# Kernel tuning notes

Hardware: AMD Instinct MI355X
Metric: run time of the kernel (lower is better)

The kernel has to match this reference:

```python
import jax, jax.numpy as jnp
import numpy as np

N_NODES = 100000
N_EDGES = 1600000
IN_F, HID, N_CLASS = 128, 128, 40


def setup_inputs() -> dict:
    key = jax.random.key(0)
    ks = jax.random.split(key, 12)
    feat = jax.random.normal(ks[0], (N_NODES, IN_F), dtype=jnp.float32)
    src = jax.random.randint(ks[1], (N_EDGES,), 0, N_NODES, dtype=jnp.int32)
    dst = jax.random.randint(ks[2], (N_EDGES,), 0, N_NODES, dtype=jnp.int32)
    s = 1.0 / np.sqrt(IN_F)
    W1_self = jax.random.uniform(ks[3], (IN_F, HID), minval=-s, maxval=s)
    W1_neigh = jax.random.uniform(ks[4], (IN_F, HID), minval=-s, maxval=s)
    b1 = jnp.zeros((HID,), jnp.float32)
    s2 = 1.0 / np.sqrt(HID)
    W2_self = jax.random.uniform(ks[5], (HID, HID), minval=-s2, maxval=s2)
    W2_neigh = jax.random.uniform(ks[6], (HID, HID), minval=-s2, maxval=s2)
    b2 = jnp.zeros((HID,), jnp.float32)
    W_score = jax.random.uniform(ks[7], (HID, N_CLASS), minval=-s2, maxval=s2)
    b_score = jax.random.uniform(ks[8], (N_CLASS,), minval=-s2, maxval=s2)
    return {"feat": feat, "src": src, "dst": dst,
            "W1_self": W1_self, "W1_neigh": W1_neigh, "b1": b1,
            "W2_self": W2_self, "W2_neigh": W2_neigh, "b2": b2,
            "W_score": W_score, "b_score": b_score}


def _mean_agg(h, src, dst, deg_inv):
    # gather -> segment-sum over destination nodes -> mean
    msg = h[src]                                              # [E, d]
    agg = jax.ops.segment_sum(msg, dst, num_segments=N_NODES)  # [N, d]
    return agg * deg_inv[:, None]


def _sage_conv(h, src, dst, deg_inv, W_self, W_neigh, b):
    h_neigh = _mean_agg(h, src, dst, deg_inv)
    return h @ W_self + h_neigh @ W_neigh + b


def reference(feat, src, dst, W1_self, W1_neigh, b1, W2_self, W2_neigh, b2, W_score, b_score):
    # dgl.add_self_loop: append (i, i) edges
    loops = jnp.arange(N_NODES, dtype=src.dtype)
    src_f = jnp.concatenate([src, loops])
    dst_f = jnp.concatenate([dst, loops])
    deg = jax.ops.segment_sum(jnp.ones_like(dst_f, dtype=feat.dtype), dst_f, num_segments=N_NODES)
    deg_inv = 1.0 / deg  # every node has a self loop -> deg >= 1
    h = _sage_conv(feat, src_f, dst_f, deg_inv, W1_self, W1_neigh, b1)
    h = jnp.where(h >= 0, h, 0.01 * h)  # LeakyReLU(0.01)
    h = _sage_conv(h, src_f, dst_f, deg_inv, W2_self, W2_neigh, b2)
    return h @ W_score + b_score
```

## Files before the change

### kernel.cpp

```cpp
#include <hip/hip_runtime.h>
#include <cstdint>
#include <cstddef>

#define N_NODES 100000
#define N_EDGES 1600000
#define FDIM 128
#define NCLS 40
#define SCAN_BLOCKS 98

#define FILL_CLASSES 8
#define FILL_BPC 256
#define FILL_EPB 6250
#define NODES_PER_CLASS (N_NODES / FILL_CLASSES)

__global__ void count_kernel(const int* __restrict__ dst, int* __restrict__ cnt, int E) {
    int e = blockIdx.x * blockDim.x + threadIdx.x;
    if (e < E) atomicAdd(&cnt[dst[e]], 1);
}

__global__ void scan_phase1(const int* __restrict__ cnt, int* __restrict__ excl,
                            int* __restrict__ bsum, float* __restrict__ deg_inv, int n) {
    __shared__ int lds[1024];
    int tid = threadIdx.x;
    int i = blockIdx.x * 1024 + tid;
    int v = (i < n) ? cnt[i] : 0;
    if (i < n) deg_inv[i] = 1.0f / (float)(v + 1);
    lds[tid] = v;
    __syncthreads();
    for (int d = 1; d < 1024; d <<= 1) {
        int t = (tid >= d) ? lds[tid - d] : 0;
        __syncthreads();
        lds[tid] += t;
        __syncthreads();
    }
    if (i < n) excl[i] = lds[tid] - v;
    if (tid == 1023) bsum[blockIdx.x] = lds[1023];
}

__global__ void scan_phase2(const int* __restrict__ bsum, int* __restrict__ boff, int nb) {
    __shared__ int lds[128];
    int tid = threadIdx.x;
    int v = (tid < nb) ? bsum[tid] : 0;
    lds[tid] = v;
    __syncthreads();
    for (int d = 1; d < 128; d <<= 1) {
        int t = (tid >= d) ? lds[tid - d] : 0;
        __syncthreads();
        lds[tid] += t;
        __syncthreads();
    }
    if (tid < nb) boff[tid] = lds[tid] - v;
    if (tid == 127) boff[nb] = lds[127];
}

__global__ void scan_phase3(const int* __restrict__ excl, const int* __restrict__ boff,
                            int* __restrict__ off, int n, int nb) {
    int i = blockIdx.x * blockDim.x + threadIdx.x;
    if (i < n) off[i] = excl[i] + boff[i >> 10];
    if (i == 0) off[n] = boff[nb];
}

__global__ __launch_bounds__(256) void fill_kernel(
        const int* __restrict__ src, const int* __restrict__ dst,
        const int* __restrict__ off, int* __restrict__ cnt,
        int* __restrict__ csr_src, int E) {
    int cls = blockIdx.x & (FILL_CLASSES - 1);
    int w   = blockIdx.x >> 3;
    int lo  = cls * NODES_PER_CLASS;
    int hi  = lo + NODES_PER_CLASS;
    int beg = w * FILL_EPB;
    int end = beg + FILL_EPB; if (end > E) end = E;
    for (int e = beg + threadIdx.x; e < end; e += 256) {
        int d = dst[e];
        if (d >= lo && d < hi) {
            int p = atomicSub(&cnt[d], 1) - 1;
            csr_src[off[d] + p] = src[e];
        }
    }
}

__global__ __launch_bounds__(256) void agg_kernel(
        const float* __restrict__ x, const int* __restrict__ csr_off,
        const int* __restrict__ csr_src, const float* __restrict__ deg_inv,
        float* __restrict__ outbuf, int N) {
    int wid = blockIdx.x * 4 + (threadIdx.x >> 6);
    int lane = threadIdx.x & 63;
    if (wid >= N) return;
    float2 acc = *((const float2*)(x + (size_t)wid * FDIM) + lane);
    int beg = csr_off[wid], end = csr_off[wid + 1];
    for (int j = beg; j < end; j += 64) {
        int c = end - j; if (c > 64) c = 64;
        int idx = (lane < c) ? csr_src[j + lane] : 0;
        int t = 0;
        for (; t + 16 <= c; t += 16) {
            float2 v[16];
#pragma unroll
            for (int u = 0; u < 16; ++u)
                v[u] = *((const float2*)(x + (size_t)__shfl(idx, t + u) * FDIM) + lane);
#pragma unroll
            for (int u = 0; u < 16; ++u) { acc.x += v[u].x; acc.y += v[u].y; }
        }
        for (; t + 4 <= c; t += 4) {
            float2 v[4];
#pragma unroll
            for (int u = 0; u < 4; ++u)
                v[u] = *((const float2*)(x + (size_t)__shfl(idx, t + u) * FDIM) + lane);
#pragma unroll
            for (int u = 0; u < 4; ++u) { acc.x += v[u].x; acc.y += v[u].y; }
        }
        for (; t < c; ++t) {
            float2 v = *((const float2*)(x + (size_t)__shfl(idx, t) * FDIM) + lane);
            acc.x += v.x; acc.y += v.y;
        }
    }
    float di = deg_inv[wid];
    float2 r; r.x = acc.x * di; r.y = acc.y * di;
    *((float2*)(outbuf + (size_t)wid * FDIM) + lane) = r;
}

__global__ __launch_bounds__(256) void gemm1_kernel(
        const float* __restrict__ feat, const float* __restrict__ agg,
        const float* __restrict__ Wself, const float* __restrict__ Wneigh,
        const float* __restrict__ bias, float* __restrict__ h1, int M) {
    __shared__ float At[32][132];
    __shared__ float Ws[32][132];
    int tid = threadIdx.x;
    int tx = tid & 15;
    int ty = tid >> 4;
    int row0 = blockIdx.x * 128;
    float acc[8][8];
#pragma unroll
    for (int i = 0; i < 8; ++i)
#pragma unroll
        for (int j = 0; j < 8; ++j) acc[i][j] = 0.f;

    for (int chunk = 0; chunk < 8; ++chunk) {
        const float* Asrc = (chunk < 4) ? feat : agg;
        const float* Wsrc = (chunk < 4) ? Wself : Wneigh;
        int kb = (chunk & 3) << 5;
        {
            int r = tid >> 1;
            int c0 = (tid & 1) << 4;
            int gr = row0 + r;
            const float* sp = Asrc + (size_t)gr * FDIM + kb + c0;
#pragma unroll
            for (int i = 0; i < 4; ++i) {
                float4 v = (gr < M) ? *(const float4*)(sp + (i << 2))
                                    : make_float4(0.f, 0.f, 0.f, 0.f);
                At[c0 + (i << 2) + 0][r] = v.x;
                At[c0 + (i << 2) + 1][r] = v.y;
                At[c0 + (i << 2) + 2][r] = v.z;
                At[c0 + (i << 2) + 3][r] = v.w;
            }
        }
        {
            int kr = tid >> 3;
            int c0 = (tid & 7) << 4;
            const float* sp = Wsrc + (size_t)(kb + kr) * FDIM + c0;
#pragma unroll
            for (int i = 0; i < 4; ++i)
                *(float4*)&Ws[kr][c0 + (i << 2)] = *(const float4*)(sp + (i << 2));
        }
        __syncthreads();
#pragma unroll 2
        for (int k = 0; k < 32; ++k) {
            float a[8], w[8];
            *(float4*)&a[0] = *(const float4*)&At[k][ty << 3];
            *(float4*)&a[4] = *(const float4*)&At[k][(ty << 3) + 4];
            *(float4*)&w[0] = *(const float4*)&Ws[k][tx << 3];
            *(float4*)&w[4] = *(const float4*)&Ws[k][(tx << 3) + 4];
#pragma unroll
            for (int i = 0; i < 8; ++i)
#pragma unroll
                for (int j = 0; j < 8; ++j)
                    acc[i][j] = fmaf(a[i], w[j], acc[i][j]);
        }
        __syncthreads();
    }
    float bcol[8];
    *(float4*)&bcol[0] = *(const float4*)&bias[tx << 3];
    *(float4*)&bcol[4] = *(const float4*)&bias[(tx << 3) + 4];
#pragma unroll
    for (int i = 0; i < 8; ++i) {
        int gr = row0 + (ty << 3) + i;
        if (gr < M) {
            float o[8];
#pragma unroll
            for (int j = 0; j < 8; ++j) {
                float v = acc[i][j] + bcol[j];
                o[j] = (v >= 0.f) ? v : 0.01f * v;
            }
            float4* dp = (float4*)(h1 + (size_t)gr * FDIM + (tx << 3));
            dp[0] = make_float4(o[0], o[1], o[2], o[3]);
            dp[1] = make_float4(o[4], o[5], o[6], o[7]);
        }
    }
}

__global__ void wfuse_kernel(const float* __restrict__ W2s, const float* __restrict__ W2n,
                             const float* __restrict__ b2, const float* __restrict__ Wsc,
                             const float* __restrict__ bsc,
                             float* __restrict__ Wf, float* __restrict__ bf) {
    int gid = blockIdx.x * blockDim.x + threadIdx.x;
    if (gid < 256 * NCLS) {
        int r = gid / NCLS, c = gid % NCLS;
        const float* wrow = (r < 128) ? (W2s + (size_t)r * 128) : (W2n + (size_t)(r - 128) * 128);
        float acc = 0.f;
        for (int k = 0; k < 128; ++k) acc = fmaf(wrow[k], Wsc[k * NCLS + c], acc);
        Wf[gid] = acc;
    } else if (gid < 256 * NCLS + NCLS) {
        int c = gid - 256 * NCLS;
        float acc = bsc[c];
        for (int k = 0; k < 128; ++k) acc = fmaf(b2[k], Wsc[k * NCLS + c], acc);
        bf[c] = acc;
    }
}

__global__ __launch_bounds__(256) void gemm2p_kernel(
        const float* __restrict__ h1, const float* __restrict__ Wf,
        float* __restrict__ pp, int M) {
    __shared__ float As[128][36];
    __shared__ float Ws2[32][84];
    int tid = threadIdx.x;
    int tx = tid & 7;
    int ty = tid >> 3;
    int row0 = blockIdx.x * 128;
    float acc[4][10];
#pragma unroll
    for (int i = 0; i < 4; ++i)
#pragma unroll
        for (int j = 0; j < 10; ++j) acc[i][j] = 0.f;

    for (int chunk = 0; chunk < 4; ++chunk) {
        int kb = chunk << 5;
        {
            int r = tid >> 1;
            int c0 = (tid & 1) << 4;
            int gr = row0 + r;
            const float* sp = h1 + (size_t)gr * FDIM + kb + c0;
#pragma unroll
            for (int i = 0; i < 4; ++i) {
                float4 v = (gr < M) ? *(const float4*)(sp + (i << 2))
                                    : make_float4(0.f, 0.f, 0.f, 0.f);
                *(float4*)&As[r][c0 + (i << 2)] = v;
            }
        }
        {
            for (int idx = tid; idx < 32 * 80; idx += 256) {
                int kr = idx / 80, c = idx % 80;
                float v = (c < NCLS) ? Wf[(kb + kr) * NCLS + c]
                                     : Wf[(128 + kb + kr) * NCLS + (c - NCLS)];
                Ws2[kr][c] = v;
            }
        }
        __syncthreads();
#pragma unroll 4
        for (int k = 0; k < 32; ++k) {
            float a[4], w[10];
#pragma unroll
            for (int i = 0; i < 4; ++i) a[i] = As[ty + (i << 5)][k];
#pragma unroll
            for (int j = 0; j < 10; ++j) w[j] = Ws2[k][tx + (j << 3)];
#pragma unroll
            for (int i = 0; i < 4; ++i)
#pragma unroll
                for (int j = 0; j < 10; ++j)
                    acc[i][j] = fmaf(a[i], w[j], acc[i][j]);
        }
        __syncthreads();
    }
#pragma unroll
    for (int i = 0; i < 4; ++i) {
        int gr = row0 + ty + (i << 5);
        if (gr < M) {
            float* dp = pp + (size_t)gr * 80 + tx;
#pragma unroll
            for (int j = 0; j < 10; ++j)
                dp[j << 3] = acc[i][j];
        }
    }
}

__global__ __launch_bounds__(256) void final_kernel(
        const float* __restrict__ pp, const int* __restrict__ csr_off,
        const int* __restrict__ csr_src, const float* __restrict__ deg_inv,
        const float* __restrict__ bf, float* __restrict__ out, int N) {
    int wid = blockIdx.x * 4 + (threadIdx.x >> 6);
    int lane = threadIdx.x & 63;
    if (wid >= N) return;
    bool act = (lane < NCLS);
    int ln = act ? lane : 0;
    float accv = act ? pp[(size_t)wid * 80 + NCLS + ln] : 0.f;
    int beg = csr_off[wid], end = csr_off[wid + 1];
    for (int j = beg; j < end; j += 64) {
        int c = end - j; if (c > 64) c = 64;
        int idx = (lane < c) ? csr_src[j + lane] : 0;
        int t = 0;
        for (; t + 16 <= c; t += 16) {
            float v[16];
#pragma unroll
            for (int u = 0; u < 16; ++u)
                v[u] = pp[(size_t)__shfl(idx, t + u) * 80 + NCLS + ln];
#pragma unroll
            for (int u = 0; u < 16; ++u) accv += v[u];
        }
        for (; t + 4 <= c; t += 4) {
            float v[4];
#pragma unroll
            for (int u = 0; u < 4; ++u)
                v[u] = pp[(size_t)__shfl(idx, t + u) * 80 + NCLS + ln];
#pragma unroll
            for (int u = 0; u < 4; ++u) accv += v[u];
        }
        for (; t < c; ++t)
            accv += pp[(size_t)__shfl(idx, t) * 80 + NCLS + ln];
    }
    if (act)
        out[(size_t)wid * NCLS + ln] = pp[(size_t)wid * 80 + ln] + bf[ln]
                                       + deg_inv[wid] * accv;
}

extern "C" void kernel_launch(void* const* d_in, const int* in_sizes, int n_in,
                              void* d_out, int out_size, void* d_ws, size_t ws_size,
                              hipStream_t stream) {
    (void)in_sizes; (void)n_in; (void)out_size; (void)ws_size;
    const float* feat = (const float*)d_in[0];
    const int*   src  = (const int*)d_in[1];
    const int*   dst  = (const int*)d_in[2];
    const float* W1s  = (const float*)d_in[3];
    const float* W1n  = (const float*)d_in[4];
    const float* b1   = (const float*)d_in[5];
    const float* W2s  = (const float*)d_in[6];
    const float* W2n  = (const float*)d_in[7];
    const float* b2   = (const float*)d_in[8];
    const float* Wsc  = (const float*)d_in[9];
    const float* bsc  = (const float*)d_in[10];
    float* out = (float*)d_out;

    char* ws = (char*)d_ws;
    float* agg     = (float*)(ws + 0);
    float* h1      = (float*)(ws + 51200000);
    float* deg_inv = (float*)(ws + 102400000);
    int*   cnt     = (int*)  (ws + 102800000);
    int*   excl    = (int*)  (ws + 103200000);
    int*   csr_off = (int*)  (ws + 103600000);
    int*   csr_src = (int*)  (ws + 104000128);
    int*   bsum    = (int*)  (ws + 110400128);
    int*   boff    = (int*)  (ws + 110400640);
    float* Wf      = (float*)(ws + 110401664);
    float* bf      = (float*)(ws + 110442624);
    float* pp      = agg;

    hipMemsetAsync(cnt, 0, N_NODES * sizeof(int), stream);

    count_kernel<<<(N_EDGES + 255) / 256, 256, 0, stream>>>(dst, cnt, N_EDGES);
    scan_phase1<<<SCAN_BLOCKS, 1024, 0, stream>>>(cnt, excl, bsum, deg_inv, N_NODES);
    scan_phase2<<<1, 128, 0, stream>>>(bsum, boff, SCAN_BLOCKS);
    scan_phase3<<<SCAN_BLOCKS, 1024, 0, stream>>>(excl, boff, csr_off, N_NODES, SCAN_BLOCKS);
    fill_kernel<<<FILL_CLASSES * FILL_BPC, 256, 0, stream>>>(src, dst, csr_off, cnt, csr_src, N_EDGES);
    wfuse_kernel<<<41, 256, 0, stream>>>(W2s, W2n, b2, Wsc, bsc, Wf, bf);

    agg_kernel<<<N_NODES / 4, 256, 0, stream>>>(feat, csr_off, csr_src, deg_inv, agg, N_NODES);
    gemm1_kernel<<<(N_NODES + 127) / 128, 256, 0, stream>>>(feat, agg, W1s, W1n, b1, h1, N_NODES);
    gemm2p_kernel<<<(N_NODES + 127) / 128, 256, 0, stream>>>(h1, Wf, pp, N_NODES);
    final_kernel<<<N_NODES / 4, 256, 0, stream>>>(pp, csr_off, csr_src, deg_inv, bf, out, N_NODES);
}
```

Baseline: 577.4 us.

## Gather fp16 copy of features in aggregation and split neighbor projection buffer

Adds a kernel that converts the input features to fp16 into spare workspace. The first-layer neighbor aggregation now gathers half-precision rows and accumulates in fp32, halving the bytes of the random gathers. The second-layer projection is written as two separate contiguous 40-wide arrays (self and neighbor) instead of one 80-wide interleaved array, so the final gather reads denser rows. The cost is an extra conversion pass over the features and a precision loss on gathered features.

```diff
diff --git a/kernel.cpp b/kernel.cpp
--- a/kernel.cpp
+++ b/kernel.cpp
@@ -1,4 +1,5 @@
 #include <hip/hip_runtime.h>
+#include <hip/hip_fp16.h>
 #include <cstdint>
 #include <cstddef>
 
@@ -16,6 +17,22 @@
 __global__ void count_kernel(const int* __restrict__ dst, int* __restrict__ cnt, int E) {
     int e = blockIdx.x * blockDim.x + threadIdx.x;
     if (e < E) atomicAdd(&cnt[dst[e]], 1);
+}
+
+__global__ __launch_bounds__(256) void feat16_kernel(
+        const float* __restrict__ feat, __half* __restrict__ feat16, int total8) {
+    int i = blockIdx.x * blockDim.x + threadIdx.x;
+    if (i < total8) {
+        const float* sp = feat + (size_t)i * 8;
+        float4 a = *(const float4*)sp;
+        float4 b = *(const float4*)(sp + 4);
+        __half h[8];
+        h[0] = __float2half_rn(a.x); h[1] = __float2half_rn(a.y);
+        h[2] = __float2half_rn(a.z); h[3] = __float2half_rn(a.w);
+        h[4] = __float2half_rn(b.x); h[5] = __float2half_rn(b.y);
+        h[6] = __float2half_rn(b.z); h[7] = __float2half_rn(b.w);
+        *(uint4*)(feat16 + (size_t)i * 8) = *(uint4*)h;
+    }
 }
 
 __global__ void scan_phase1(const int* __restrict__ cnt, int* __restrict__ excl,
@@ -80,9 +97,9 @@
 }
 
 __global__ __launch_bounds__(256) void agg_kernel(
-        const float* __restrict__ x, const int* __restrict__ csr_off,
-        const int* __restrict__ csr_src, const float* __restrict__ deg_inv,
-        float* __restrict__ outbuf, int N) {
+        const float* __restrict__ x, const __half* __restrict__ x16,
+        const int* __restrict__ csr_off, const int* __restrict__ csr_src,
+        const float* __restrict__ deg_inv, float* __restrict__ outbuf, int N) {
     int wid = blockIdx.x * 4 + (threadIdx.x >> 6);
     int lane = threadIdx.x & 63;
     if (wid >= N) return;
@@ -93,24 +110,31 @@
         int idx = (lane < c) ? csr_src[j + lane] : 0;
         int t = 0;
         for (; t + 16 <= c; t += 16) {
-            float2 v[16];
+            __half2 v[16];
 #pragma unroll
             for (int u = 0; u < 16; ++u)
-                v[u] = *((const float2*)(x + (size_t)__shfl(idx, t + u) * FDIM) + lane);
-#pragma unroll
-            for (int u = 0; u < 16; ++u) { acc.x += v[u].x; acc.y += v[u].y; }
+                v[u] = *((const __half2*)(x16 + (size_t)__shfl(idx, t + u) * FDIM) + lane);
+#pragma unroll
+            for (int u = 0; u < 16; ++u) {
+                float2 f = __half22float2(v[u]);
+                acc.x += f.x; acc.y += f.y;
+            }
         }
         for (; t + 4 <= c; t += 4) {
-            float2 v[4];
+            __half2 v[4];
 #pragma unroll
             for (int u = 0; u < 4; ++u)
-                v[u] = *((const float2*)(x + (size_t)__shfl(idx, t + u) * FDIM) + lane);
-#pragma unroll
-            for (int u = 0; u < 4; ++u) { acc.x += v[u].x; acc.y += v[u].y; }
+                v[u] = *((const __half2*)(x16 + (size_t)__shfl(idx, t + u) * FDIM) + lane);
+#pragma unroll
+            for (int u = 0; u < 4; ++u) {
+                float2 f = __half22float2(v[u]);
+                acc.x += f.x; acc.y += f.y;
+            }
         }
         for (; t < c; ++t) {
-            float2 v = *((const float2*)(x + (size_t)__shfl(idx, t) * FDIM) + lane);
-            acc.x += v.x; acc.y += v.y;
+            float2 f = __half22float2(
+                *((const __half2*)(x16 + (size_t)__shfl(idx, t) * FDIM) + lane));
+            acc.x += f.x; acc.y += f.y;
         }
     }
     float di = deg_inv[wid];
@@ -218,7 +242,7 @@
 
 __global__ __launch_bounds__(256) void gemm2p_kernel(
         const float* __restrict__ h1, const float* __restrict__ Wf,
-        float* __restrict__ pp, int M) {
+        float* __restrict__ ps, float* __restrict__ pn, int M) {
     __shared__ float As[128][36];
     __shared__ float Ws2[32][84];
     int tid = threadIdx.x;
@@ -273,24 +297,27 @@
     for (int i = 0; i < 4; ++i) {
         int gr = row0 + ty + (i << 5);
         if (gr < M) {
-            float* dp = pp + (size_t)gr * 80 + tx;
-#pragma unroll
-            for (int j = 0; j < 10; ++j)
-                dp[j << 3] = acc[i][j];
+#pragma unroll
+            for (int j = 0; j < 10; ++j) {
+                int cj = tx + (j << 3);
+                if (cj < NCLS) ps[(size_t)gr * NCLS + cj] = acc[i][j];
+                else           pn[(size_t)gr * NCLS + (cj - NCLS)] = acc[i][j];
+            }
         }
     }
 }
 
 __global__ __launch_bounds__(256) void final_kernel(
-        const float* __restrict__ pp, const int* __restrict__ csr_off,
-        const int* __restrict__ csr_src, const float* __restrict__ deg_inv,
-        const float* __restrict__ bf, float* __restrict__ out, int N) {
+        const float* __restrict__ ps, const float* __restrict__ pn,
+        const int* __restrict__ csr_off, const int* __restrict__ csr_src,
+        const float* __restrict__ deg_inv, const float* __restrict__ bf,
+        float* __restrict__ out, int N) {
     int wid = blockIdx.x * 4 + (threadIdx.x >> 6);
     int lane = threadIdx.x & 63;
     if (wid >= N) return;
     bool act = (lane < NCLS);
     int ln = act ? lane : 0;
-    float accv = act ? pp[(size_t)wid * 80 + NCLS + ln] : 0.f;
+    float accv = act ? pn[(size_t)wid * NCLS + ln] : 0.f;
     int beg = csr_off[wid], end = csr_off[wid + 1];
     for (int j = beg; j < end; j += 64) {
         int c = end - j; if (c > 64) c = 64;
@@ -300,7 +327,7 @@
             float v[16];
 #pragma unroll
             for (int u = 0; u < 16; ++u)
-                v[u] = pp[(size_t)__shfl(idx, t + u) * 80 + NCLS + ln];
+                v[u] = pn[(size_t)__shfl(idx, t + u) * NCLS + ln];
 #pragma unroll
             for (int u = 0; u < 16; ++u) accv += v[u];
         }
@@ -308,15 +335,15 @@
             float v[4];
 #pragma unroll
             for (int u = 0; u < 4; ++u)
-                v[u] = pp[(size_t)__shfl(idx, t + u) * 80 + NCLS + ln];
+                v[u] = pn[(size_t)__shfl(idx, t + u) * NCLS + ln];
 #pragma unroll
             for (int u = 0; u < 4; ++u) accv += v[u];
         }
         for (; t < c; ++t)
-            accv += pp[(size_t)__shfl(idx, t) * 80 + NCLS + ln];
+            accv += pn[(size_t)__shfl(idx, t) * NCLS + ln];
     }
     if (act)
-        out[(size_t)wid * NCLS + ln] = pp[(size_t)wid * 80 + ln] + bf[ln]
+        out[(size_t)wid * NCLS + ln] = ps[(size_t)wid * NCLS + ln] + bf[ln]
                                        + deg_inv[wid] * accv;
 }
 
@@ -338,21 +365,25 @@
     float* out = (float*)d_out;
 
     char* ws = (char*)d_ws;
-    float* agg     = (float*)(ws + 0);
-    float* h1      = (float*)(ws + 51200000);
-    float* deg_inv = (float*)(ws + 102400000);
-    int*   cnt     = (int*)  (ws + 102800000);
-    int*   excl    = (int*)  (ws + 103200000);
-    int*   csr_off = (int*)  (ws + 103600000);
-    int*   csr_src = (int*)  (ws + 104000128);
-    int*   bsum    = (int*)  (ws + 110400128);
-    int*   boff    = (int*)  (ws + 110400640);
-    float* Wf      = (float*)(ws + 110401664);
-    float* bf      = (float*)(ws + 110442624);
-    float* pp      = agg;
+    float*  agg     = (float*)(ws + 0);
+    float*  h1      = (float*)(ws + 51200000);
+    float*  deg_inv = (float*)(ws + 102400000);
+    int*    cnt     = (int*)  (ws + 102800000);
+    int*    excl    = (int*)  (ws + 103200000);
+    int*    csr_off = (int*)  (ws + 103600000);
+    int*    csr_src = (int*)  (ws + 104000128);
+    int*    bsum    = (int*)  (ws + 110400128);
+    int*    boff    = (int*)  (ws + 110400640);
+    float*  Wf      = (float*)(ws + 110401664);
+    float*  bf      = (float*)(ws + 110442624);
+    __half* feat16  = (__half*)h1;
+    float*  ps      = agg;
+    float*  pn      = (float*)(ws + 16000000);
 
     hipMemsetAsync(cnt, 0, N_NODES * sizeof(int), stream);
 
+    feat16_kernel<<<(N_NODES * FDIM / 8 + 255) / 256, 256, 0, stream>>>(
+        feat, feat16, N_NODES * FDIM / 8);
     count_kernel<<<(N_EDGES + 255) / 256, 256, 0, stream>>>(dst, cnt, N_EDGES);
     scan_phase1<<<SCAN_BLOCKS, 1024, 0, stream>>>(cnt, excl, bsum, deg_inv, N_NODES);
     scan_phase2<<<1, 128, 0, stream>>>(bsum, boff, SCAN_BLOCKS);
@@ -360,8 +391,10 @@
     fill_kernel<<<FILL_CLASSES * FILL_BPC, 256, 0, stream>>>(src, dst, csr_off, cnt, csr_src, N_EDGES);
     wfuse_kernel<<<41, 256, 0, stream>>>(W2s, W2n, b2, Wsc, bsc, Wf, bf);
 
-    agg_kernel<<<N_NODES / 4, 256, 0, stream>>>(feat, csr_off, csr_src, deg_inv, agg, N_NODES);
+    agg_kernel<<<N_NODES / 4, 256, 0, stream>>>(feat, feat16, csr_off, csr_src,
+                                                deg_inv, agg, N_NODES);
     gemm1_kernel<<<(N_NODES + 127) / 128, 256, 0, stream>>>(feat, agg, W1s, W1n, b1, h1, N_NODES);
-    gemm2p_kernel<<<(N_NODES + 127) / 128, 256, 0, stream>>>(h1, Wf, pp, N_NODES);
-    final_kernel<<<N_NODES / 4, 256, 0, stream>>>(pp, csr_off, csr_src, deg_inv, bf, out, N_NODES);
-}
+    gemm2p_kernel<<<(N_NODES + 127) / 128, 256, 0, stream>>>(h1, Wf, ps, pn, N_NODES);
+    final_kernel<<<N_NODES / 4, 256, 0, stream>>>(ps, pn, csr_off, csr_src,
+                                                  deg_inv, bf, out, N_NODES);
+}
```

After: 531.5 us. 1.09x faster.
